# Kernel tuning notes

Measured on AMD Instinct MI355X. Metric: run time of the kernel, lower is better.

## Reference

```python
import jax, jax.numpy as jnp
import numpy as np

N = 20000      # nodes
E = 320000     # edges per metapath graph
M = 3          # metapaths
IN = 256       # input feat dim
HID = 64       # num_hidden per head
NH = 4         # nhead (layer 1)
OUT = 256      # out_dim
NHO = 1        # nhead_out (layer 2)
SA_H = 128     # semantic attention hidden
NEG_SLOPE = 0.2


def gat_conv(h, W, attn_l, attn_r, src, dst, apply_relu):
    # h: [N, F_in]; W: [F_in, H*D]; attn_l/attn_r: [H, D]
    H, D = attn_l.shape
    feat = (h @ W).reshape(N, H, D)                      # [N, H, D]
    el = jnp.sum(feat * attn_l, axis=-1)                 # [N, H]
    er = jnp.sum(feat * attn_r, axis=-1)                 # [N, H]
    e = jax.nn.leaky_relu(el[src] + er[dst], NEG_SLOPE)  # [E, H]
    # edge softmax grouped by destination node
    emax = jax.ops.segment_max(e, dst, num_segments=N)   # [N, H] (-inf for empty)
    emax = jnp.where(jnp.isfinite(emax), emax, 0.0)
    ee = jnp.exp(e - emax[dst])                          # [E, H]
    denom = jax.ops.segment_sum(ee, dst, num_segments=N) # [N, H]
    alpha = ee / (denom[dst] + 1e-9)                     # [E, H]
    msg = alpha[:, :, None] * feat[src]                  # [E, H, D]
    out = jax.ops.segment_sum(msg, dst, num_segments=N)  # [N, H, D]
    out = out.reshape(N, H * D)                          # concat heads
    return jax.nn.relu(out) if apply_relu else out


def semantic_attention(z, W1, b1, v):
    # z: [N, M, F]
    w = jnp.tanh(z @ W1 + b1) @ v          # [N, M, 1]
    w = w.mean(axis=0)                     # [M, 1]
    beta = jax.nn.softmax(w, axis=0)       # [M, 1]
    out = jnp.sum(beta[None, :, :] * z, axis=1)  # [N, F]
    att_mp = beta.squeeze()                # [M]
    return out, att_mp


def setup_inputs() -> dict:
    key = jax.random.key(0)
    ks = jax.random.split(key, 16)
    s = 0.05
    return {
        "x": jax.random.normal(ks[0], (N, IN), dtype=jnp.float32),
        "edges": jax.random.randint(ks[1], (M, 2, E), 0, N, dtype=jnp.int64)
                 if jax.config.jax_enable_x64 else
                 jax.random.randint(ks[1], (M, 2, E), 0, N, dtype=jnp.int32),
        "W1": jax.random.normal(ks[2], (IN, NH * HID), dtype=jnp.float32) * s,
        "al1": jax.random.normal(ks[3], (NH, HID), dtype=jnp.float32) * s,
        "ar1": jax.random.normal(ks[4], (NH, HID), dtype=jnp.float32) * s,
        "saW1": jax.random.normal(ks[5], (NH * HID, SA_H), dtype=jnp.float32) * s,
        "sab1": jnp.zeros((SA_H,), dtype=jnp.float32),
        "sav1": jax.random.normal(ks[6], (SA_H, 1), dtype=jnp.float32) * s,
        "W2": jax.random.normal(ks[7], (NH * HID, NHO * OUT), dtype=jnp.float32) * s,
        "al2": jax.random.normal(ks[8], (NHO, OUT), dtype=jnp.float32) * s,
        "ar2": jax.random.normal(ks[9], (NHO, OUT), dtype=jnp.float32) * s,
        "saW2": jax.random.normal(ks[10], (NHO * OUT, SA_H), dtype=jnp.float32) * s,
        "sab2": jnp.zeros((SA_H,), dtype=jnp.float32),
        "sav2": jax.random.normal(ks[11], (SA_H, 1), dtype=jnp.float32) * s,
    }


def reference(x, edges, W1, al1, ar1, saW1, sab1, sav1,
              W2, al2, ar2, saW2, sab2, sav2):
    h = x
    # HAN layer 1: shared GATConv over each metapath graph, relu activation
    z = jnp.stack([gat_conv(h, W1, al1, ar1, edges[i, 0], edges[i, 1], True)
                   for i in range(M)], axis=1)          # [N, M, NH*HID]
    h, att_mp = semantic_attention(z, saW1, sab1, sav1)
    # HAN layer 2: last layer, no activation (encoding=False)
    z = jnp.stack([gat_conv(h, W2, al2, ar2, edges[i, 0], edges[i, 1], False)
                   for i in range(M)], axis=1)          # [N, M, NHO*OUT]
    h, att_mp = semantic_attention(z, saW2, sab2, sav2)
    return h, att_mp
```

## Files before the change

kernel.cpp:

```cpp
#include <hip/hip_runtime.h>
#include <hip/hip_bf16.h>
#include <math.h>

#define NN 20000
#define EE 320000
#define MM 3
#define FW 256
#define SAH 128
#define NB 79
#define RNG 2500

typedef __attribute__((ext_vector_type(8))) short bf16x8;
typedef __attribute__((ext_vector_type(4))) float f32x4;

static __device__ __forceinline__ float lrelu(float x){ return x > 0.f ? x : 0.2f*x; }

static __device__ __forceinline__ unsigned short f2bf(float f) {
    unsigned u = __float_as_uint(f);
    return (unsigned short)((u + 0x7FFFu + ((u >> 16) & 1u)) >> 16);
}
static __device__ __forceinline__ float bf2f(unsigned short b) {
    return __uint_as_float(((unsigned)b) << 16);
}
static __device__ __forceinline__ float bflo(unsigned u){ return __uint_as_float(u << 16); }
static __device__ __forceinline__ float bfhi(unsigned u){ return __uint_as_float(u & 0xffff0000u); }
static __device__ __forceinline__ unsigned pk2bf(float lo, float hi) {
    return ((unsigned)f2bf(lo)) | (((unsigned)f2bf(hi)) << 16);
}

#define XBLK 2500
#define ZBLK 235
__global__ __launch_bounds__(256) void prep_kernel(const float* __restrict__ x, unsigned short* __restrict__ xb,
                                                   const float* __restrict__ W1, unsigned short* __restrict__ W1t,
                                                   const float* __restrict__ saW1, unsigned short* __restrict__ saW1t,
                                                   const float* __restrict__ W2, unsigned short* __restrict__ W2t,
                                                   const float* __restrict__ saW2, unsigned short* __restrict__ saW2t,
                                                   int* __restrict__ cnt, float* __restrict__ wsum) {
    int b = blockIdx.x, tid = threadIdx.x;
    if (b < XBLK) {
        int i = b*256 + tid;
        const float4* p = (const float4*)x + (size_t)i*2;
        float4 v0 = p[0], v1 = p[1];
        uint4 o;
        o.x = pk2bf(v0.x, v0.y); o.y = pk2bf(v0.z, v0.w);
        o.z = pk2bf(v1.x, v1.y); o.w = pk2bf(v1.z, v1.w);
        ((uint4*)xb)[i] = o;
        return;
    }
    int b2 = b - XBLK;
    if (b2 < 256)      { int n = b2;       W1t  [(size_t)n*256 + tid] = f2bf(W1  [(size_t)tid*256 + n]); return; }
    else if (b2 < 384) { int n = b2 - 256; saW1t[(size_t)n*256 + tid] = f2bf(saW1[(size_t)tid*SAH + n]); return; }
    else if (b2 < 640) { int n = b2 - 384; W2t  [(size_t)n*256 + tid] = f2bf(W2  [(size_t)tid*256 + n]); return; }
    else if (b2 < 768) { int n = b2 - 640; saW2t[(size_t)n*256 + tid] = f2bf(saW2[(size_t)tid*SAH + n]); return; }
    int zb = b2 - 768;
    int i = zb*256 + tid;
    if (i < MM*NN) cnt[i] = 0;
    if (zb == 0 && tid < 8) wsum[tid] = 0.f;
}

__global__ __launch_bounds__(256) void hist_kernel(const int* __restrict__ edges, int* __restrict__ cnt) {
    int idx = blockIdx.x*256 + threadIdx.x;
    if (idx >= MM*EE/4) return;
    int m = idx / (EE/4), e4 = idx - m*(EE/4);
    int4 d = ((const int4*)(edges + (size_t)(m*2+1)*EE))[e4];
    atomicAdd(&cnt[m*NN + d.x], 1);
    atomicAdd(&cnt[m*NN + d.y], 1);
    atomicAdd(&cnt[m*NN + d.z], 1);
    atomicAdd(&cnt[m*NN + d.w], 1);
}

__global__ __launch_bounds__(256) void scanA_kernel(const int* __restrict__ cnt, int* __restrict__ rowptr, int* __restrict__ bsum) {
    int m = blockIdx.y;
    int i = blockIdx.x*256 + threadIdx.x;
    int v = (i < NN) ? cnt[m*NN + i] : 0;
    int lane = threadIdx.x & 63;
    int val = v;
    #pragma unroll
    for (int o = 1; o < 64; o <<= 1) { int t = __shfl_up(val, o); if (lane >= o) val += t; }
    __shared__ int ws[4];
    int w = threadIdx.x >> 6;
    if (lane == 63) ws[w] = val;
    __syncthreads();
    #pragma unroll
    for (int j = 0; j < 3; ++j) if (j < w) val += ws[j];
    if (i < NN) rowptr[m*(NN+1) + 1 + i] = val;
    if (threadIdx.x == 255) bsum[m*NB + blockIdx.x] = val;
}

__global__ __launch_bounds__(128) void scanB_kernel(const int* __restrict__ bsum, int* __restrict__ boff) {
    __shared__ int s[128];
    int t = threadIdx.x;
    for (int m = 0; m < MM; ++m) {
        int v = (t < NB) ? bsum[m*NB + t] : 0;
        s[t] = v; __syncthreads();
        for (int o = 1; o < 128; o <<= 1) {
            int x = (t >= o) ? s[t - o] : 0;
            __syncthreads();
            s[t] += x;
            __syncthreads();
        }
        if (t < NB) boff[m*NB + t] = s[t] - v;
        __syncthreads();
    }
}

__global__ __launch_bounds__(256) void scanC_kernel(const int* __restrict__ cnt, int* __restrict__ rowptr,
                                                    const int* __restrict__ boff, int* __restrict__ cursor) {
    int m = blockIdx.y;
    int i = blockIdx.x*256 + threadIdx.x;
    if (i >= NN) return;
    int incl = rowptr[m*(NN+1) + 1 + i] + boff[m*NB + blockIdx.x];
    rowptr[m*(NN+1) + 1 + i] = incl;
    cursor[m*NN + i] = incl - cnt[m*NN + i];
    if (i == 0 && blockIdx.x == 0) rowptr[m*(NN+1)] = 0;
}

__global__ __launch_bounds__(256) void scatter_kernel(const int* __restrict__ edges, int* __restrict__ cursor,
                                                      uint2* __restrict__ csr) {
    int m = blockIdx.y;
    int r = blockIdx.x & 7;
    int chunk = blockIdx.x >> 3;
    int e4 = chunk*256 + threadIdx.x;
    if (e4 >= EE/4) return;
    int lo = r * RNG, hi = lo + RNG;
    int4 s = ((const int4*)(edges + (size_t)(m*2  )*EE))[e4];
    int4 d = ((const int4*)(edges + (size_t)(m*2+1)*EE))[e4];
    if (d.x >= lo && d.x < hi) { int p = atomicAdd(&cursor[m*NN + d.x], 1); csr[(size_t)m*EE + p] = make_uint2((unsigned)s.x, (unsigned)d.x); }
    if (d.y >= lo && d.y < hi) { int p = atomicAdd(&cursor[m*NN + d.y], 1); csr[(size_t)m*EE + p] = make_uint2((unsigned)s.y, (unsigned)d.y); }
    if (d.z >= lo && d.z < hi) { int p = atomicAdd(&cursor[m*NN + d.z], 1); csr[(size_t)m*EE + p] = make_uint2((unsigned)s.z, (unsigned)d.z); }
    if (d.w >= lo && d.w < hi) { int p = atomicAdd(&cursor[m*NN + d.w], 1); csr[(size_t)m*EE + p] = make_uint2((unsigned)s.w, (unsigned)d.w); }
}

template<int H>
__global__ __launch_bounds__(256) void gemm_mfma_kernel(const unsigned short* __restrict__ A,
                                                        const unsigned short* __restrict__ Bt,
                                                        const float* __restrict__ attl, const float* __restrict__ attr,
                                                        unsigned short* __restrict__ C,
                                                        float* __restrict__ el, float* __restrict__ er) {
    int tid = threadIdx.x;
    int w = tid >> 6, lane = tid & 63;
    int rowgrp = w & 1, half = w >> 1;
    int r0 = blockIdx.x*32 + rowgrp*16;
    int colbase = half * 128;
    int lrow = lane & 15, lk = lane >> 4;

    bf16x8 a[8];
    const unsigned short* ap = A + (size_t)(r0 + lrow)*256 + lk*8;
    #pragma unroll
    for (int k = 0; k < 8; ++k) a[k] = *(const bf16x8*)(ap + k*32);

    float pelv[2][4] = {{0.f,0.f,0.f,0.f},{0.f,0.f,0.f,0.f}};
    float perv[2][4] = {{0.f,0.f,0.f,0.f},{0.f,0.f,0.f,0.f}};

    #pragma unroll
    for (int n = 0; n < 8; ++n) {
        int col0 = colbase + n*16;
        const unsigned short* bp = Bt + (size_t)(col0 + lrow)*256 + lk*8;
        f32x4 acc = {0.f, 0.f, 0.f, 0.f};
        #pragma unroll
        for (int k = 0; k < 8; ++k) {
            bf16x8 bfr = *(const bf16x8*)(bp + k*32);
            acc = __builtin_amdgcn_mfma_f32_16x16x32_bf16(a[k], bfr, acc, 0, 0, 0);
        }
        int col = col0 + lrow;
        float al = attl[col], ar = attr[col];
        int hl = (H == 4) ? (n >> 2) : 0;
        #pragma unroll
        for (int r = 0; r < 4; ++r) {
            float cv = acc[r];
            pelv[hl][r] += cv * al;
            perv[hl][r] += cv * ar;
            C[(size_t)(r0 + lk*4 + r)*256 + col] = f2bf(cv);
        }
    }

    int nhl = (H == 4) ? 2 : 1;
    #pragma unroll
    for (int hl = 0; hl < 2; ++hl) {
        if (hl >= nhl) break;
        #pragma unroll
        for (int r = 0; r < 4; ++r) {
            float pe = pelv[hl][r], pr = perv[hl][r];
            #pragma unroll
            for (int o = 1; o < 16; o <<= 1) { pe += __shfl_xor(pe, o); pr += __shfl_xor(pr, o); }
            pelv[hl][r] = pe; perv[hl][r] = pr;
        }
    }

    if (H == 4) {
        if (lrow == 0) {
            int row = r0 + lk*4;
            #pragma unroll
            for (int hl = 0; hl < 2; ++hl) {
                int head = half*2 + hl;
                #pragma unroll
                for (int r = 0; r < 4; ++r) {
                    el[(size_t)(row + r)*4 + head] = pelv[hl][r];
                    er[(size_t)(row + r)*4 + head] = perv[hl][r];
                }
            }
        }
    } else {
        __shared__ float elds[2][32], erds[2][32];
        if (lrow == 0) {
            int rib = rowgrp*16 + lk*4;
            #pragma unroll
            for (int r = 0; r < 4; ++r) {
                elds[half][rib + r] = pelv[0][r];
                erds[half][rib + r] = perv[0][r];
            }
        }
        __syncthreads();
        if (tid < 32) {
            el[blockIdx.x*32 + tid] = elds[0][tid] + elds[1][tid];
            er[blockIdx.x*32 + tid] = erds[0][tid] + erds[1][tid];
        }
    }
}

template<int H>
__global__ __launch_bounds__(256) void edge_ee_kernel(const unsigned long long* __restrict__ csr_ull,
                                                      const float* __restrict__ el, const float* __restrict__ er,
                                                      unsigned short* __restrict__ ee16) {
    int idx = blockIdx.x*256 + threadIdx.x;
    if (idx >= MM*EE/2) return;
    unsigned long long p0 = csr_ull[(size_t)idx*2];
    unsigned long long p1 = csr_ull[(size_t)idx*2 + 1];
    unsigned s0 = (unsigned)p0, d0 = (unsigned)(p0 >> 32);
    unsigned s1 = (unsigned)p1, d1 = (unsigned)(p1 >> 32);
    if (H == 4) {
        float4 l0 = *(const float4*)&el[s0*4];
        float4 r0 = *(const float4*)&er[d0*4];
        float4 l1 = *(const float4*)&el[s1*4];
        float4 r1 = *(const float4*)&er[d1*4];
        uint4 o;
        o.x = pk2bf(expf(lrelu(l0.x + r0.x)), expf(lrelu(l0.y + r0.y)));
        o.y = pk2bf(expf(lrelu(l0.z + r0.z)), expf(lrelu(l0.w + r0.w)));
        o.z = pk2bf(expf(lrelu(l1.x + r1.x)), expf(lrelu(l1.y + r1.y)));
        o.w = pk2bf(expf(lrelu(l1.z + r1.z)), expf(lrelu(l1.w + r1.w)));
        *(uint4*)&ee16[(size_t)idx*8] = o;
    } else {
        unsigned o = pk2bf(expf(lrelu(el[s0] + er[d0])), expf(lrelu(el[s1] + er[d1])));
        *(unsigned*)&ee16[(size_t)idx*2] = o;
    }
}

template<int H, bool RELU>
__global__ __launch_bounds__(256) void agg_kernel(const unsigned short* __restrict__ feat,
                                                  const unsigned short* __restrict__ ee16,
                                                  const int* __restrict__ rowptr,
                                                  const unsigned* __restrict__ csr_u,
                                                  unsigned short* __restrict__ z) {
    int m = blockIdx.y;
    int tid = threadIdx.x;
    int lane = tid & 63, wv = tid >> 6;
    int n = blockIdx.x * 4 + wv;
    int eslot = lane >> 5, flane = lane & 31;
    int h = (H == 4) ? (flane >> 3) : 0;
    int beg = rowptr[m*(NN+1) + n], end = rowptr[m*(NN+1) + n + 1];
    const size_t eb = (size_t)m*EE;

    float a[8] = {};
    float den = 0.f;

    int e = beg + eslot;
    unsigned sA = 0, sB = 0;
    float wA = 0.f, wB = 0.f;
    if (e     < end) { sA = csr_u[(eb+e  )*2]; wA = (H==4)? bf2f(ee16[(eb+e  )*4+h]) : bf2f(ee16[eb+e  ]); }
    if (e + 2 < end) { sB = csr_u[(eb+e+2)*2]; wB = (H==4)? bf2f(ee16[(eb+e+2)*4+h]) : bf2f(ee16[eb+e+2]); }

    while (e < end) {
        uint4 v0 = *(const uint4*)(feat + (size_t)sA*256 + flane*8);
        bool h1 = (e + 2 < end);
        uint4 v1 = make_uint4(0,0,0,0);
        if (h1) v1 = *(const uint4*)(feat + (size_t)sB*256 + flane*8);
        float w0 = wA, w1 = h1 ? wB : 0.f;
        if (e + 4 < end) { sA = csr_u[(eb+e+4)*2]; wA = (H==4)? bf2f(ee16[(eb+e+4)*4+h]) : bf2f(ee16[eb+e+4]); }
        if (e + 6 < end) { sB = csr_u[(eb+e+6)*2]; wB = (H==4)? bf2f(ee16[(eb+e+6)*4+h]) : bf2f(ee16[eb+e+6]); }
        den += w0 + w1;
        a[0] += w0*bflo(v0.x) + w1*bflo(v1.x);
        a[1] += w0*bfhi(v0.x) + w1*bfhi(v1.x);
        a[2] += w0*bflo(v0.y) + w1*bflo(v1.y);
        a[3] += w0*bfhi(v0.y) + w1*bfhi(v1.y);
        a[4] += w0*bflo(v0.z) + w1*bflo(v1.z);
        a[5] += w0*bfhi(v0.z) + w1*bfhi(v1.z);
        a[6] += w0*bflo(v0.w) + w1*bflo(v1.w);
        a[7] += w0*bfhi(v0.w) + w1*bfhi(v1.w);
        e += 4;
    }

    #pragma unroll
    for (int j = 0; j < 8; ++j) a[j] += __shfl_xor(a[j], 32);
    den += __shfl_xor(den, 32);

    if (eslot == 0) {
        float inv = 1.f / (den + 1e-9f);
        #pragma unroll
        for (int j = 0; j < 8; ++j) {
            a[j] *= inv;
            if (RELU) a[j] = fmaxf(a[j], 0.f);
        }
        uint4 pk;
        pk.x = pk2bf(a[0], a[1]);
        pk.y = pk2bf(a[2], a[3]);
        pk.z = pk2bf(a[4], a[5]);
        pk.w = pk2bf(a[6], a[7]);
        *(uint4*)&z[((size_t)n*MM + m)*256 + flane*8] = pk;
    }
}

__global__ __launch_bounds__(256) void semw_mfma_kernel(const unsigned short* __restrict__ Z,
                                                        const unsigned short* __restrict__ Wt,
                                                        const float* __restrict__ bias, const float* __restrict__ v,
                                                        float* __restrict__ wsum) {
    int tid = threadIdx.x;
    int w = tid >> 6, lane = tid & 63;
    int r0 = blockIdx.x*64 + w*16;
    int lrow = lane & 15, lk = lane >> 4;

    int arow = r0 + lrow;
    if (arow >= NN*MM) arow = NN*MM - 1;
    bf16x8 a[8];
    const unsigned short* ap = Z + (size_t)arow*256 + lk*8;
    #pragma unroll
    for (int k = 0; k < 8; ++k) a[k] = *(const bf16x8*)(ap + k*32);

    float p[4] = {0.f, 0.f, 0.f, 0.f};
    #pragma unroll
    for (int n = 0; n < 8; ++n) {
        int col = n*16 + lrow;
        const unsigned short* bp = Wt + (size_t)col*256 + lk*8;
        f32x4 acc = {0.f, 0.f, 0.f, 0.f};
        #pragma unroll
        for (int k = 0; k < 8; ++k) {
            bf16x8 bfr = *(const bf16x8*)(bp + k*32);
            acc = __builtin_amdgcn_mfma_f32_16x16x32_bf16(a[k], bfr, acc, 0, 0, 0);
        }
        float bb = bias[col], vv = v[col];
        #pragma unroll
        for (int r = 0; r < 4; ++r)
            p[r] += tanhf(acc[r] + bb) * vv;
    }

    #pragma unroll
    for (int r = 0; r < 4; ++r) {
        #pragma unroll
        for (int o = 1; o < 16; o <<= 1) p[r] += __shfl_xor(p[r], o);
    }

    __shared__ float loc[3];
    if (tid < 3) loc[tid] = 0.f;
    __syncthreads();
    if (lrow == 0) {
        #pragma unroll
        for (int r = 0; r < 4; ++r) {
            int row = r0 + lk*4 + r;
            if (row < NN*MM) atomicAdd(&loc[row % MM], p[r]);
        }
    }
    __syncthreads();
    if (tid < 3) atomicAdd(&wsum[tid], loc[tid]);
}

__global__ __launch_bounds__(128) void combine_bf16_kernel(const unsigned short* __restrict__ z, const float* __restrict__ wsum,
                                                           unsigned short* __restrict__ outb) {
    __shared__ float bs[3];
    int n = blockIdx.x, t = threadIdx.x;
    if (t == 0) {
        float w0 = wsum[0] / (float)NN, w1 = wsum[1] / (float)NN, w2 = wsum[2] / (float)NN;
        float mx = fmaxf(w0, fmaxf(w1, w2));
        float e0 = expf(w0 - mx), e1 = expf(w1 - mx), e2 = expf(w2 - mx);
        float s = e0 + e1 + e2;
        bs[0] = e0 / s; bs[1] = e1 / s; bs[2] = e2 / s;
    }
    __syncthreads();
    float b0 = bs[0], b1 = bs[1], b2 = bs[2];
    size_t base = (size_t)n*MM*256 + t*2;
    unsigned z0 = *(const unsigned*)&z[base];
    unsigned z1 = *(const unsigned*)&z[base + 256];
    unsigned z2 = *(const unsigned*)&z[base + 512];
    float ox = b0*bflo(z0) + b1*bflo(z1) + b2*bflo(z2);
    float oy = b0*bfhi(z0) + b1*bfhi(z1) + b2*bfhi(z2);
    *(unsigned*)&outb[(size_t)n*256 + t*2] = pk2bf(ox, oy);
}

__global__ __launch_bounds__(128) void combine_kernel(const unsigned short* __restrict__ z, const float* __restrict__ wsum,
                                                      float* __restrict__ out, float* __restrict__ att_out) {
    __shared__ float bs[3];
    int n = blockIdx.x, t = threadIdx.x;
    if (t == 0) {
        float w0 = wsum[0] / (float)NN, w1 = wsum[1] / (float)NN, w2 = wsum[2] / (float)NN;
        float mx = fmaxf(w0, fmaxf(w1, w2));
        float e0 = expf(w0 - mx), e1 = expf(w1 - mx), e2 = expf(w2 - mx);
        float s = e0 + e1 + e2;
        bs[0] = e0 / s; bs[1] = e1 / s; bs[2] = e2 / s;
        if (n == 0) { att_out[0] = bs[0]; att_out[1] = bs[1]; att_out[2] = bs[2]; }
    }
    __syncthreads();
    float b0 = bs[0], b1 = bs[1], b2 = bs[2];
    size_t base = (size_t)n*MM*256 + t*2;
    unsigned z0 = *(const unsigned*)&z[base];
    unsigned z1 = *(const unsigned*)&z[base + 256];
    unsigned z2 = *(const unsigned*)&z[base + 512];
    float2 o;
    o.x = b0*bflo(z0) + b1*bflo(z1) + b2*bflo(z2);
    o.y = b0*bfhi(z0) + b1*bfhi(z1) + b2*bfhi(z2);
    *(float2*)&out[(size_t)n*256 + t*2] = o;
}

extern "C" void kernel_launch(void* const* d_in, const int* in_sizes, int n_in,
                              void* d_out, int out_size, void* d_ws, size_t ws_size,
                              hipStream_t stream) {
    const float* x    = (const float*)d_in[0];
    const int*   edges= (const int*)  d_in[1];
    const float* W1   = (const float*)d_in[2];
    const float* al1  = (const float*)d_in[3];
    const float* ar1  = (const float*)d_in[4];
    const float* saW1 = (const float*)d_in[5];
    const float* sab1 = (const float*)d_in[6];
    const float* sav1 = (const float*)d_in[7];
    const float* W2   = (const float*)d_in[8];
    const float* al2  = (const float*)d_in[9];
    const float* ar2  = (const float*)d_in[10];
    const float* saW2 = (const float*)d_in[11];
    const float* sab2 = (const float*)d_in[12];
    const float* sav2 = (const float*)d_in[13];
    float* out = (float*)d_out;

    char* ws = (char*)d_ws;
    size_t off = 0;
    auto alloc = [&](size_t bytes) { void* p = ws + off; off += (bytes + 255) & ~(size_t)255; return p; };
    unsigned short* feat  = (unsigned short*)alloc((size_t)NN*256*2);
    unsigned short* z     = (unsigned short*)alloc((size_t)NN*MM*256*2);
    unsigned short* xb    = (unsigned short*)alloc((size_t)NN*256*2);
    unsigned short* W1t   = (unsigned short*)alloc(256*256*2);
    unsigned short* saW1t = (unsigned short*)alloc(SAH*256*2);
    unsigned short* W2t   = (unsigned short*)alloc(256*256*2);
    unsigned short* saW2t = (unsigned short*)alloc(SAH*256*2);
    unsigned short* ee16  = (unsigned short*)alloc((size_t)MM*EE*4*2);
    float* el     = (float*)alloc(NN*4*4);
    float* er     = (float*)alloc(NN*4*4);
    float* wsum   = (float*)alloc(256);
    int*   cnt    = (int*)alloc(MM*NN*4);
    int*   cursor = (int*)alloc(MM*NN*4);
    int*   rowptr = (int*)alloc(MM*(NN+1)*4);
    uint2* csr    = (uint2*)alloc((size_t)MM*EE*8);
    int*   bsum   = (int*)alloc(MM*NB*4);
    int*   boff   = (int*)alloc(MM*NB*4);
    unsigned short* hb = xb;

    int egrid2 = (MM*EE/2 + 255)/256;
    int egrid4 = (MM*EE/4 + 255)/256;
    int chunks = (EE/4 + 255)/256;
    dim3 sg(NB, MM);

    prep_kernel<<<XBLK + 768 + ZBLK, 256, 0, stream>>>(x, xb, W1, W1t, saW1, saW1t, W2, W2t, saW2, saW2t, cnt, wsum);

    hist_kernel<<<egrid4, 256, 0, stream>>>(edges, cnt);
    scanA_kernel<<<sg, 256, 0, stream>>>(cnt, rowptr, bsum);
    scanB_kernel<<<1, 128, 0, stream>>>(bsum, boff);
    scanC_kernel<<<sg, 256, 0, stream>>>(cnt, rowptr, boff, cursor);
    scatter_kernel<<<dim3(chunks*8, MM), 256, 0, stream>>>(edges, cursor, csr);

    gemm_mfma_kernel<4><<<NN/32, 256, 0, stream>>>(xb, W1t, al1, ar1, feat, el, er);
    edge_ee_kernel<4><<<egrid2, 256, 0, stream>>>((const unsigned long long*)csr, el, er, ee16);
    agg_kernel<4, true><<<dim3(NN/4, MM), 256, 0, stream>>>(feat, ee16, rowptr, (const unsigned*)csr, z);
    semw_mfma_kernel<<<(NN*MM + 63)/64, 256, 0, stream>>>(z, saW1t, sab1, sav1, wsum);
    combine_bf16_kernel<<<NN, 128, 0, stream>>>(z, wsum, hb);

    gemm_mfma_kernel<1><<<NN/32, 256, 0, stream>>>(hb, W2t, al2, ar2, feat, el, er);
    edge_ee_kernel<1><<<egrid2, 256, 0, stream>>>((const unsigned long long*)csr, el, er, ee16);
    agg_kernel<1, false><<<dim3(NN/4, MM), 256, 0, stream>>>(feat, ee16, rowptr, (const unsigned*)csr, z);
    semw_mfma_kernel<<<(NN*MM + 63)/64, 256, 0, stream>>>(z, saW2t, sab2, sav2, wsum + 4);
    combine_kernel<<<NN, 128, 0, stream>>>(z, wsum + 4, out, out + (size_t)NN*256);
}
```

Measured before the change: 389.4 us.

## Range-partition histogram atomics and use packed float2 accumulation in aggregation

The degree histogram now launches eight blocks per edge chunk. Each block only counts destinations within its own 2500-node range, so the atomics from a block land in a localized region of the count array, which is meant to improve atomic locality in cache. The cost is that every edge tile is read eight times. Separately, the aggregation kernel accumulates into float2 vectors so the compiler can emit packed FMA instructions, which may change the floating-point summation order slightly.

```diff
diff --git a/kernel.cpp b/kernel.cpp
--- a/kernel.cpp
+++ b/kernel.cpp
@@ -12,6 +12,7 @@
 
 typedef __attribute__((ext_vector_type(8))) short bf16x8;
 typedef __attribute__((ext_vector_type(4))) float f32x4;
+typedef __attribute__((ext_vector_type(2))) float f32x2;
 
 static __device__ __forceinline__ float lrelu(float x){ return x > 0.f ? x : 0.2f*x; }
 
@@ -59,14 +60,17 @@
 }
 
 __global__ __launch_bounds__(256) void hist_kernel(const int* __restrict__ edges, int* __restrict__ cnt) {
-    int idx = blockIdx.x*256 + threadIdx.x;
-    if (idx >= MM*EE/4) return;
-    int m = idx / (EE/4), e4 = idx - m*(EE/4);
+    int m = blockIdx.y;
+    int r = blockIdx.x & 7;
+    int chunk = blockIdx.x >> 3;
+    int e4 = chunk*256 + threadIdx.x;
+    if (e4 >= EE/4) return;
+    int lo = r * RNG, hi = lo + RNG;
     int4 d = ((const int4*)(edges + (size_t)(m*2+1)*EE))[e4];
-    atomicAdd(&cnt[m*NN + d.x], 1);
-    atomicAdd(&cnt[m*NN + d.y], 1);
-    atomicAdd(&cnt[m*NN + d.z], 1);
-    atomicAdd(&cnt[m*NN + d.w], 1);
+    if (d.x >= lo && d.x < hi) atomicAdd(&cnt[m*NN + d.x], 1);
+    if (d.y >= lo && d.y < hi) atomicAdd(&cnt[m*NN + d.y], 1);
+    if (d.z >= lo && d.z < hi) atomicAdd(&cnt[m*NN + d.z], 1);
+    if (d.w >= lo && d.w < hi) atomicAdd(&cnt[m*NN + d.w], 1);
 }
 
 __global__ __launch_bounds__(256) void scanA_kernel(const int* __restrict__ cnt, int* __restrict__ rowptr, int* __restrict__ bsum) {
@@ -260,7 +264,7 @@
     int beg = rowptr[m*(NN+1) + n], end = rowptr[m*(NN+1) + n + 1];
     const size_t eb = (size_t)m*EE;
 
-    float a[8] = {};
+    f32x2 a2[4] = {{0.f,0.f},{0.f,0.f},{0.f,0.f},{0.f,0.f}};
     float den = 0.f;
 
     int e = beg + eslot;
@@ -278,33 +282,37 @@
         if (e + 4 < end) { sA = csr_u[(eb+e+4)*2]; wA = (H==4)? bf2f(ee16[(eb+e+4)*4+h]) : bf2f(ee16[eb+e+4]); }
         if (e + 6 < end) { sB = csr_u[(eb+e+6)*2]; wB = (H==4)? bf2f(ee16[(eb+e+6)*4+h]) : bf2f(ee16[eb+e+6]); }
         den += w0 + w1;
-        a[0] += w0*bflo(v0.x) + w1*bflo(v1.x);
-        a[1] += w0*bfhi(v0.x) + w1*bfhi(v1.x);
-        a[2] += w0*bflo(v0.y) + w1*bflo(v1.y);
-        a[3] += w0*bfhi(v0.y) + w1*bfhi(v1.y);
-        a[4] += w0*bflo(v0.z) + w1*bflo(v1.z);
-        a[5] += w0*bfhi(v0.z) + w1*bfhi(v1.z);
-        a[6] += w0*bflo(v0.w) + w1*bflo(v1.w);
-        a[7] += w0*bfhi(v0.w) + w1*bfhi(v1.w);
+        f32x2 f;
+        f.x = bflo(v0.x); f.y = bfhi(v0.x); a2[0] += w0 * f;
+        f.x = bflo(v0.y); f.y = bfhi(v0.y); a2[1] += w0 * f;
+        f.x = bflo(v0.z); f.y = bfhi(v0.z); a2[2] += w0 * f;
+        f.x = bflo(v0.w); f.y = bfhi(v0.w); a2[3] += w0 * f;
+        f.x = bflo(v1.x); f.y = bfhi(v1.x); a2[0] += w1 * f;
+        f.x = bflo(v1.y); f.y = bfhi(v1.y); a2[1] += w1 * f;
+        f.x = bflo(v1.z); f.y = bfhi(v1.z); a2[2] += w1 * f;
+        f.x = bflo(v1.w); f.y = bfhi(v1.w); a2[3] += w1 * f;
         e += 4;
     }
 
     #pragma unroll
-    for (int j = 0; j < 8; ++j) a[j] += __shfl_xor(a[j], 32);
+    for (int j = 0; j < 4; ++j) {
+        a2[j].x += __shfl_xor(a2[j].x, 32);
+        a2[j].y += __shfl_xor(a2[j].y, 32);
+    }
     den += __shfl_xor(den, 32);
 
     if (eslot == 0) {
         float inv = 1.f / (den + 1e-9f);
         #pragma unroll
-        for (int j = 0; j < 8; ++j) {
-            a[j] *= inv;
-            if (RELU) a[j] = fmaxf(a[j], 0.f);
+        for (int j = 0; j < 4; ++j) {
+            a2[j] *= inv;
+            if (RELU) { a2[j].x = fmaxf(a2[j].x, 0.f); a2[j].y = fmaxf(a2[j].y, 0.f); }
         }
         uint4 pk;
-        pk.x = pk2bf(a[0], a[1]);
-        pk.y = pk2bf(a[2], a[3]);
-        pk.z = pk2bf(a[4], a[5]);
-        pk.w = pk2bf(a[6], a[7]);
+        pk.x = pk2bf(a2[0].x, a2[0].y);
+        pk.y = pk2bf(a2[1].x, a2[1].y);
+        pk.z = pk2bf(a2[2].x, a2[2].y);
+        pk.w = pk2bf(a2[3].x, a2[3].y);
         *(uint4*)&z[((size_t)n*MM + m)*256 + flane*8] = pk;
     }
 }
@@ -450,13 +458,12 @@
     unsigned short* hb = xb;
 
     int egrid2 = (MM*EE/2 + 255)/256;
-    int egrid4 = (MM*EE/4 + 255)/256;
     int chunks = (EE/4 + 255)/256;
     dim3 sg(NB, MM);
 
     prep_kernel<<<XBLK + 768 + ZBLK, 256, 0, stream>>>(x, xb, W1, W1t, saW1, saW1t, W2, W2t, saW2, saW2t, cnt, wsum);
 
-    hist_kernel<<<egrid4, 256, 0, stream>>>(edges, cnt);
+    hist_kernel<<<dim3(chunks*8, MM), 256, 0, stream>>>(edges, cnt);
     scanA_kernel<<<sg, 256, 0, stream>>>(cnt, rowptr, bsum);
     scanB_kernel<<<1, 128, 0, stream>>>(bsum, boff);
     scanC_kernel<<<sg, 256, 0, stream>>>(cnt, rowptr, boff, cursor);
```

Result: no change. 396.8 us (+1.9%).
